# Optimization experiments

Hardware: AMD Instinct MI355X
Metric: run time of the kernel (lower is better)

## Reference

```python
import jax, jax.numpy as jnp
import numpy as np

B, N, M = 64, 8192, 128
EPS = 1e-16
COS_EPS = 1e-8  # torch F.cosine_similarity denominator clamp


def setup_inputs() -> dict:
    key = jax.random.key(0)
    ks = jax.random.split(key, 9)
    memory = jax.random.normal(ks[0], (B, N, M), jnp.float32) * 0.1
    k = jax.random.normal(ks[1], (B, M), jnp.float32)
    beta = jax.random.uniform(ks[2], (B, 1), jnp.float32) * 5.0
    g = jax.random.uniform(ks[3], (B, 1), jnp.float32)
    s = jax.nn.softmax(jax.random.uniform(ks[4], (B, 3), jnp.float32), axis=-1)
    gamma = 1.0 + 2.0 * jax.random.uniform(ks[5], (B, 1), jnp.float32)
    w_prev = jax.random.uniform(ks[6], (B, N), jnp.float32)
    w_prev = w_prev / jnp.sum(w_prev, axis=1, keepdims=True)
    e = jax.random.uniform(ks[7], (B, M), jnp.float32)  # erase gate in [0,1]
    a = jax.random.normal(ks[8], (B, M), jnp.float32)
    return {"memory": memory, "k": k, "beta": beta, "g": g, "s": s,
            "gamma": gamma, "w_prev": w_prev, "e": e, "a": a}


def _ntm_step(memory, k, beta, g, s, gamma, w_prev, e, a):
    # --- content addressing: cosine similarity + softmax (sec 3.3.1) ---
    mem = memory + EPS                     # [B,N,M]
    kk = k[:, None, :] + EPS               # [B,1,M]
    dot = jnp.einsum('bnm,bom->bn', mem, kk)
    denom = (jnp.maximum(jnp.linalg.norm(mem, axis=-1), COS_EPS)
             * jnp.maximum(jnp.linalg.norm(kk, axis=-1), COS_EPS))
    w_r = jax.nn.softmax(beta * (dot / denom), axis=1)       # [B,N]
    # --- interpolation with previous weighting ---
    w_g = g * w_r + (1.0 - g) * w_prev
    # --- circular 3-tap shift (cross-correlation, as torch conv1d) ---
    # c[i] = s0*w[i-1] + s1*w[i] + s2*w[i+1]
    w_s = (s[:, 0:1] * jnp.roll(w_g, 1, axis=1)
           + s[:, 1:2] * w_g
           + s[:, 2:3] * jnp.roll(w_g, -1, axis=1))
    # --- sharpen ---
    w_pow = w_s ** gamma
    w = w_pow / (jnp.sum(w_pow, axis=1, keepdims=True) + EPS)  # [B,N]
    # --- read (sec 3.1) ---
    read = jnp.einsum('bn,bnm->bm', w, memory)
    # --- write: erase then add via rank-1 outer products (sec 3.2) ---
    erase = w[:, :, None] * e[:, None, :]                      # [B,N,M]
    add = w[:, :, None] * a[:, None, :]
    new_memory = memory * (1.0 - erase) + add
    return read, w, new_memory


def reference(memory, k, beta, g, s, gamma, w_prev, e, a):
    return _ntm_step(memory, k, beta, g, s, gamma, w_prev, e, a)
```

## Files before the change

kernel.cpp:

```cpp
#include <hip/hip_runtime.h>
#include <math.h>

#define Bb 64
#define Nn 8192
#define Mm 128
#define EPSf 1e-16f
#define COS_EPSf 1e-8f

typedef __attribute__((ext_vector_type(4))) float f32x4;

#define SITERS 8
__global__ __launch_bounds__(256) void score_kernel(
    const float* __restrict__ memory, const float* __restrict__ k,
    const float* __restrict__ beta, float* score ) {
  const int b = blockIdx.y;
  const int tid = threadIdx.x;
  const int q = tid & 15;
  const int rsub = tid >> 4;
  const int row0 = blockIdx.x * (16 * SITERS);
  const size_t bbase = (size_t)b * Nn;

  const f32x4 ka = *(const f32x4*)(k + b * Mm + q * 4);
  const f32x4 kb = *(const f32x4*)(k + b * Mm + 64 + q * 4);
  float kf[8];
#pragma unroll
  for (int j = 0; j < 4; j++) { kf[j] = ka[j] + EPSf; kf[4 + j] = kb[j] + EPSf; }
  float sqk = 0.f;
#pragma unroll
  for (int j = 0; j < 8; j++) sqk += kf[j] * kf[j];
  sqk += __shfl_xor(sqk, 1); sqk += __shfl_xor(sqk, 2);
  sqk += __shfl_xor(sqk, 4); sqk += __shfl_xor(sqk, 8);
  const float bscale = beta[b] / fmaxf(sqrtf(sqk), COS_EPSf);

#pragma unroll 4
  for (int it = 0; it < SITERS; it++) {
    const int row = row0 + it * 16 + rsub;
    const float* rp = memory + (bbase + row) * Mm;
    const f32x4 ma = *(const f32x4*)(rp + q * 4);
    const f32x4 mb = *(const f32x4*)(rp + 64 + q * 4);
    float dot = 0.f, sqm = 0.f;
#pragma unroll
    for (int j = 0; j < 4; j++) {
      const float m0 = ma[j] + EPSf, m1 = mb[j] + EPSf;
      dot = fmaf(m0, kf[j], dot); dot = fmaf(m1, kf[4 + j], dot);
      sqm = fmaf(m0, m0, sqm);    sqm = fmaf(m1, m1, sqm);
    }
    dot += __shfl_xor(dot, 1); sqm += __shfl_xor(sqm, 1);
    dot += __shfl_xor(dot, 2); sqm += __shfl_xor(sqm, 2);
    dot += __shfl_xor(dot, 4); sqm += __shfl_xor(sqm, 4);
    dot += __shfl_xor(dot, 8); sqm += __shfl_xor(sqm, 8);
    if (q == 0) score[bbase + row] = bscale * dot / fmaxf(sqrtf(sqm), COS_EPSf);
  }
}

__device__ __forceinline__ float block_sum16(float v, float* scratch) {
  const int lane = threadIdx.x & 63, wid = threadIdx.x >> 6;
  for (int o = 32; o; o >>= 1) v += __shfl_down(v, o);
  if (lane == 0) scratch[wid] = v;
  __syncthreads();
  if (threadIdx.x < 16) {
    v = scratch[threadIdx.x];
    for (int o = 8; o; o >>= 1) v += __shfl_down(v, o);
    if (threadIdx.x == 0) scratch[0] = v;
  }
  __syncthreads();
  v = scratch[0];
  __syncthreads();
  return v;
}

__device__ __forceinline__ float block_max16(float v, float* scratch) {
  const int lane = threadIdx.x & 63, wid = threadIdx.x >> 6;
  for (int o = 32; o; o >>= 1) v = fmaxf(v, __shfl_down(v, o));
  if (lane == 0) scratch[wid] = v;
  __syncthreads();
  if (threadIdx.x < 16) {
    v = scratch[threadIdx.x];
    for (int o = 8; o; o >>= 1) v = fmaxf(v, __shfl_down(v, o));
    if (threadIdx.x == 0) scratch[0] = v;
  }
  __syncthreads();
  v = scratch[0];
  __syncthreads();
  return v;
}

__global__ __launch_bounds__(1024) void weight_kernel(
    const float* score,
    const float* __restrict__ w_prev, const float* __restrict__ g,
    const float* __restrict__ s, const float* __restrict__ gamma,
    float* w_out) {
  __shared__ float wg[Nn];
  __shared__ float scratch[16];
  const int b = blockIdx.x;
  const int tid = threadIdx.x;
  const int PT = Nn / 1024;

  float sc[PT];
  float lmax = -INFINITY;
#pragma unroll
  for (int i = 0; i < PT; i++) {
    sc[i] = score[b * Nn + tid + i * 1024];
    lmax = fmaxf(lmax, sc[i]);
  }
  const float bmax = block_max16(lmax, scratch);

  float lsum = 0.f;
#pragma unroll
  for (int i = 0; i < PT; i++) {
    sc[i] = expf(sc[i] - bmax);
    lsum += sc[i];
  }
  const float Z = block_sum16(lsum, scratch);
  const float invZ = 1.f / Z;

  const float gb = g[b];
  const float s0 = s[b * 3 + 0], s1 = s[b * 3 + 1], s2 = s[b * 3 + 2];
  const float gam = gamma[b];

#pragma unroll
  for (int i = 0; i < PT; i++) {
    const int n = tid + i * 1024;
    const float wr = sc[i] * invZ;
    wg[n] = gb * wr + (1.f - gb) * w_prev[b * Nn + n];
  }
  __syncthreads();

  float wp[PT];
  float psum = 0.f;
#pragma unroll
  for (int i = 0; i < PT; i++) {
    const int n = tid + i * 1024;
    const float wsv = s0 * wg[(n + Nn - 1) & (Nn - 1)] + s1 * wg[n] + s2 * wg[(n + 1) & (Nn - 1)];
    wp[i] = powf(wsv, gam);
    psum += wp[i];
  }
  const float S = block_sum16(psum, scratch) + EPSf;
  const float invS = 1.f / S;
#pragma unroll
  for (int i = 0; i < PT; i++) w_out[b * Nn + tid + i * 1024] = wp[i] * invS;
}

template <bool ATOMIC>
__global__ __launch_bounds__(256) void rw_kernel(
    const float* __restrict__ memory, const float* __restrict__ w,
    const float* __restrict__ e, const float* __restrict__ a,
    float* __restrict__ new_memory, float* __restrict__ out) {
  const int CH = 256;
  const int b = blockIdx.x >> 5;
  const int chunk = blockIdx.x & 31;
  const int tid = threadIdx.x;
  const int m4 = tid & 31;
  const int rowg = tid >> 5;

  const f32x4 e4 = *(const f32x4*)(e + b * Mm + m4 * 4);
  const f32x4 a4 = *(const f32x4*)(a + b * Mm + m4 * 4);
  f32x4 acc = {0.f, 0.f, 0.f, 0.f};
  const size_t bbase = (size_t)b * Nn;
  const int row0 = chunk * CH;

#pragma unroll 8
  for (int i = 0; i < CH / 8; i++) {
    const int n = row0 + i * 8 + rowg;
    const float wn = w[bbase + n];
    const f32x4 mv = *(const f32x4*)(memory + (bbase + n) * Mm + m4 * 4);
    const f32x4 nm = mv + wn * (a4 - e4 * mv);
    __builtin_nontemporal_store(nm, (f32x4*)(new_memory + (bbase + n) * Mm + m4 * 4));
    acc += wn * mv;
  }

  __shared__ f32x4 red[256];
  red[tid] = acc;
  __syncthreads();
  for (int sh = 128; sh >= 32; sh >>= 1) {
    if (tid < sh) {
      const f32x4 o = red[tid + sh];
      red[tid] += o;
    }
    __syncthreads();
  }
  if (tid < 32) {
    const f32x4 r = red[tid];
    if (ATOMIC) {
      atomicAdd(&out[b * Mm + tid * 4 + 0], r[0]);
      atomicAdd(&out[b * Mm + tid * 4 + 1], r[1]);
      atomicAdd(&out[b * Mm + tid * 4 + 2], r[2]);
      atomicAdd(&out[b * Mm + tid * 4 + 3], r[3]);
    } else {
      *(f32x4*)(out + ((size_t)(b * 32 + chunk) * Mm) + tid * 4) = r;
    }
  }
}

__global__ __launch_bounds__(256) void reduce_read_kernel(
    const float* __restrict__ partial, float* __restrict__ readout) {
  const int t = blockIdx.x * 256 + threadIdx.x;
  const int b = t >> 7, m = t & 127;
  const float* p = partial + (size_t)b * 32 * Mm + m;
  float sum = 0.f;
#pragma unroll
  for (int c = 0; c < 32; c++) sum += p[c * Mm];
  readout[t] = sum;
}

extern "C" void kernel_launch(void* const* d_in, const int* in_sizes, int n_in,
                              void* d_out, int out_size, void* d_ws, size_t ws_size,
                              hipStream_t stream) {
  const float* memory = (const float*)d_in[0];
  const float* k      = (const float*)d_in[1];
  const float* beta   = (const float*)d_in[2];
  const float* g      = (const float*)d_in[3];
  const float* s      = (const float*)d_in[4];
  const float* gamma  = (const float*)d_in[5];
  const float* w_prev = (const float*)d_in[6];
  const float* e      = (const float*)d_in[7];
  const float* a      = (const float*)d_in[8];

  float* out      = (float*)d_out;
  float* read_out = out;
  float* w_out    = out + Bb * Mm;
  float* new_mem  = out + Bb * Mm + (size_t)Bb * Nn;
  float* score    = w_out;
  float* partial  = (float*)d_ws;

  dim3 sgrid(Nn / (16 * SITERS), Bb);
  score_kernel<<<sgrid, 256, 0, stream>>>(memory, k, beta, score);
  weight_kernel<<<Bb, 1024, 0, stream>>>(score, w_prev, g, s, gamma, w_out);
  const size_t need = (size_t)Bb * 32 * Mm * sizeof(float);
  if (ws_size >= need) {
    rw_kernel<false><<<Bb * 32, 256, 0, stream>>>(memory, w_out, e, a, new_mem, partial);
    reduce_read_kernel<<<(Bb * Mm) / 256, 256, 0, stream>>>(partial, read_out);
  } else {
    hipMemsetAsync(read_out, 0, (size_t)Bb * Mm * sizeof(float), stream);
    rw_kernel<true><<<Bb * 32, 256, 0, stream>>>(memory, w_out, e, a, new_mem, read_out);
  }
}
```

Measured before the change: 153.9 us.

## Fuse read reduction into rw kernel via last-block ticket counter

Each read-write block writes its partial read vector, then takes a per-batch ticket through an atomic counter, and the last block sums the 32 partials, which removes the separate reduce kernel launch. The counters are zeroed with a memset before the launch. The score loop is fully unrolled, and the new-memory store becomes a regular store instead of a nontemporal one. The atomic fallback for small workspaces is removed, and a memset launch is added.

```diff
diff --git a/kernel.cpp b/kernel.cpp
--- a/kernel.cpp
+++ b/kernel.cpp
@@ -32,7 +32,7 @@
   sqk += __shfl_xor(sqk, 4); sqk += __shfl_xor(sqk, 8);
   const float bscale = beta[b] / fmaxf(sqrtf(sqk), COS_EPSf);
 
-#pragma unroll 4
+#pragma unroll 8
   for (int it = 0; it < SITERS; it++) {
     const int row = row0 + it * 16 + rsub;
     const float* rp = memory + (bbase + row) * Mm;
@@ -141,11 +141,12 @@
   for (int i = 0; i < PT; i++) w_out[b * Nn + tid + i * 1024] = wp[i] * invS;
 }
 
-template <bool ATOMIC>
+template <bool FUSED>
 __global__ __launch_bounds__(256) void rw_kernel(
     const float* __restrict__ memory, const float* __restrict__ w,
     const float* __restrict__ e, const float* __restrict__ a,
-    float* __restrict__ new_memory, float* __restrict__ out) {
+    float* __restrict__ new_memory, float* partial,
+    unsigned int* counters, float* __restrict__ read_out) {
   const int CH = 256;
   const int b = blockIdx.x >> 5;
   const int chunk = blockIdx.x & 31;
@@ -165,7 +166,7 @@
     const float wn = w[bbase + n];
     const f32x4 mv = *(const f32x4*)(memory + (bbase + n) * Mm + m4 * 4);
     const f32x4 nm = mv + wn * (a4 - e4 * mv);
-    __builtin_nontemporal_store(nm, (f32x4*)(new_memory + (bbase + n) * Mm + m4 * 4));
+    *(f32x4*)(new_memory + (bbase + n) * Mm + m4 * 4) = nm;
     acc += wn * mv;
   }
 
@@ -180,14 +181,25 @@
     __syncthreads();
   }
   if (tid < 32) {
-    const f32x4 r = red[tid];
-    if (ATOMIC) {
-      atomicAdd(&out[b * Mm + tid * 4 + 0], r[0]);
-      atomicAdd(&out[b * Mm + tid * 4 + 1], r[1]);
-      atomicAdd(&out[b * Mm + tid * 4 + 2], r[2]);
-      atomicAdd(&out[b * Mm + tid * 4 + 3], r[3]);
-    } else {
-      *(f32x4*)(out + ((size_t)(b * 32 + chunk) * Mm) + tid * 4) = r;
+    *(f32x4*)(partial + ((size_t)(b * 32 + chunk) * Mm) + tid * 4) = red[tid];
+  }
+
+  if (FUSED) {
+    __shared__ unsigned int ticket;
+    if (tid < 64) {
+      __threadfence();
+      if (tid == 0) ticket = atomicAdd(&counters[b], 1u);
+    }
+    __syncthreads();
+    if (ticket == 31u) {
+      __threadfence();
+      if (tid < Mm) {
+        const float* p = partial + (size_t)b * 32 * Mm + tid;
+        float sum = 0.f;
+#pragma unroll
+        for (int c = 0; c < 32; c++) sum += p[c * Mm];
+        read_out[b * Mm + tid] = sum;
+      }
     }
   }
 }
@@ -222,16 +234,20 @@
   float* new_mem  = out + Bb * Mm + (size_t)Bb * Nn;
   float* score    = w_out;
   float* partial  = (float*)d_ws;
+  const size_t partial_bytes = (size_t)Bb * 32 * Mm * sizeof(float);
+  unsigned int* counters = (unsigned int*)((char*)d_ws + partial_bytes);
 
   dim3 sgrid(Nn / (16 * SITERS), Bb);
   score_kernel<<<sgrid, 256, 0, stream>>>(memory, k, beta, score);
   weight_kernel<<<Bb, 1024, 0, stream>>>(score, w_prev, g, s, gamma, w_out);
-  const size_t need = (size_t)Bb * 32 * Mm * sizeof(float);
-  if (ws_size >= need) {
-    rw_kernel<false><<<Bb * 32, 256, 0, stream>>>(memory, w_out, e, a, new_mem, partial);
+
+  if (ws_size >= partial_bytes + Bb * sizeof(unsigned int)) {
+    hipMemsetAsync(counters, 0, Bb * sizeof(unsigned int), stream);
+    rw_kernel<true><<<Bb * 32, 256, 0, stream>>>(memory, w_out, e, a, new_mem,
+                                                 partial, counters, read_out);
+  } else if (ws_size >= partial_bytes) {
+    rw_kernel<false><<<Bb * 32, 256, 0, stream>>>(memory, w_out, e, a, new_mem,
+                                                  partial, nullptr, nullptr);
     reduce_read_kernel<<<(Bb * Mm) / 256, 256, 0, stream>>>(partial, read_out);
-  } else {
-    hipMemsetAsync(read_out, 0, (size_t)Bb * Mm * sizeof(float), stream);
-    rw_kernel<true><<<Bb * 32, 256, 0, stream>>>(memory, w_out, e, a, new_mem, read_out);
-  }
-}
+  }
+}
```

Result: slower. 361.7 us (+135.1%).
